# Kernel tuning notes

Hardware: AMD Instinct MI355X
Metric: run time of the kernel (lower is better)

Reference implementation:

```python
import jax, jax.numpy as jnp
import numpy as np

# Dims: N batch, I input channels, C = in/hidden/attention/projection/out channels (all 128),
# streams=1, groups=1, spatial kernel 3, dropout 0.
N, I, C, H, W = 8, 128, 128, 36, 36


def _conv(x, w, pad):
    # x: [N, Cin, H, W], w: [Cout, Cin, kh, kw]
    return jax.lax.conv_general_dilated(
        x, w, (1, 1), pad, dimension_numbers=("NCHW", "OIHW", "NCHW"))


def _bias(b):
    return b[None, :, None, None]


def setup_inputs() -> dict:
    key = jax.random.key(0)
    ks = jax.random.split(key, 16)
    std = 0.05

    def w(k, o, i, s):
        return jax.random.normal(k, (o, i, s, s), jnp.float32) * std

    p = {}
    p["inp"] = jax.random.normal(ks[0], (N, I, H, W), jnp.float32)
    p["c0"] = jax.random.normal(ks[1], (1, C, 1, 1), jnp.float32)
    # proj_x: 1x1 conv input->in_channels, bias init 0
    p["w_x"] = w(ks[2], C, I, 1)
    p["b_x"] = jnp.zeros((C,), jnp.float32)
    # token convs (3x3, no bias); q uses SAME pad, k/v VALID
    p["w_qx"] = w(ks[3], C, C, 3)
    p["w_qc"] = w(ks[4], C, C, 3)
    scale = C ** (-0.5)  # gain = attn_channels^-0.5 on k projections
    p["w_kx"] = w(ks[5], C, C, 3) * scale
    p["w_kc"] = w(ks[6], C, C, 3) * scale
    p["w_vx"] = w(ks[7], C, C, 3)
    p["w_vc"] = w(ks[8], C, C, 3)
    # gating 1x1 convs: proj_z (bias=init_gate=1), proj_n (bias=0), in 2*proj channels
    p["w_z"] = w(ks[9], C, 2 * C, 1)
    p["b_z"] = jnp.ones((C,), jnp.float32)
    p["w_n"] = w(ks[10], C, 2 * C, 1)
    p["b_n"] = jnp.zeros((C,), jnp.float32)
    # proj_h: in_channels + 2*projection_channels -> hidden
    p["w_h"] = w(ks[11], C, 3 * C, 1)
    p["b_h"] = jnp.zeros((C,), jnp.float32)
    # output 1x1 conv hidden -> out_channels
    p["w_o"] = w(ks[12], C, C, 1)
    p["b_o"] = jnp.zeros((C,), jnp.float32)
    return p


def reference(inp, c0, w_x, b_x, w_qx, w_qc, w_kx, w_kc, w_vx, w_vc,
              w_z, b_z, w_n, b_n, w_h, b_h, w_o, b_o):
    # proj_x (1x1) -> x: [N, C, H, W]
    x = _conv(inp, w_x, "VALID") + _bias(b_x)
    n_, _, hh, ww = x.shape
    c = jnp.broadcast_to(c0, (n_, c0.shape[1], hh, ww))
    q_len = hh * ww
    # q: SAME pad -> Q = H*W tokens; k/v: VALID -> D = (H-2)*(W-2) tokens
    q = jnp.stack([_conv(x, w_qx, "SAME"), _conv(c, w_qc, "SAME")], 0)
    q = q.reshape(2, n_, -1, q_len)                      # [A, N, C, Q]
    k_x = _conv(x, w_kx, "VALID")
    d_len = k_x.shape[2] * k_x.shape[3]
    k = jnp.stack([k_x, _conv(c, w_kc, "VALID")], 0).reshape(2, n_, -1, d_len)   # [B, N, C, D]
    v = jnp.stack([_conv(x, w_vx, "VALID"), _conv(c, w_vc, "VALID")], 0)
    v = v.reshape(2, n_, -1, d_len)                      # [B, N, C, D]
    # all (A query source) x (B key/value source) attention pairs
    attn = jax.nn.softmax(jnp.einsum("ancq,bncd->anbqd", q, k), axis=-1)
    a = jnp.einsum("bncd,anbqd->anbcq", v, attn)         # [A, N, B, C, Q]
    a = a.reshape(2, n_, -1, hh, ww)                     # channels = B*C = 2*proj
    a_x, a_c = a[0], a[1]
    # GRU-style gated cell update (stored state; not part of the returned output)
    z = jax.nn.sigmoid(_conv(a_c, w_z, "VALID") + _bias(b_z))
    n_cand = jnp.tanh(_conv(a_c, w_n, "VALID") + _bias(b_n))
    c_new = z * c + (1.0 - z) * n_cand  # noqa: F841 (past['c'] in the original)
    # hidden: tanh(proj_h(cat[x, a_x])), dropout p=0 is identity
    xa = jnp.concatenate([x, a_x], axis=1)               # [N, 3*C, H, W]
    h = jnp.tanh(_conv(xa, w_h, "VALID") + _bias(b_h))
    return _conv(h, w_o, "VALID") + _bias(b_o)           # [N, C, H, W]
```

## Files before the change

### kernel.cpp

```cpp
#include <hip/hip_runtime.h>
#include <hip/hip_bf16.h>
#include <math.h>

#define NN 8
#define CH 128
#define HH 36
#define WWI 36
#define PP 1296
#define DD 1156
#define VP 1280
#define KC 1152
#define QT 81
#define DT 10

typedef __attribute__((ext_vector_type(8))) short short8;
typedef __attribute__((ext_vector_type(4))) float f32x4;

__device__ inline unsigned short f2bf(float f) {
    __hip_bfloat16 h = __float2bfloat16(f);
    return __builtin_bit_cast(unsigned short, h);
}
__device__ inline float fast_tanh(float x) {
    float e = __expf(2.f * x);
    return 1.f - 2.f / (e + 1.f);
}
#define MFMA(a, b, c) __builtin_amdgcn_mfma_f32_16x16x32_bf16((a), (b), (c), 0, 0, 0)

__global__ void k_setup(const float* __restrict__ wq, const float* __restrict__ wk,
                        const float* __restrict__ wv, const float* __restrict__ wh,
                        const float* __restrict__ wo, const float* __restrict__ wx,
                        const float* __restrict__ c0, const float* __restrict__ w_vc,
                        const float* __restrict__ b_h,
                        unsigned short* __restrict__ wcat, unsigned short* __restrict__ whb,
                        unsigned short* __restrict__ wob, unsigned short* __restrict__ wxb,
                        float* __restrict__ hconst)
{
    if (blockIdx.x == 576) {
        __shared__ float vc[CH];
        int c = threadIdx.x;
        if (c < CH) {
            float s = 0.f;
            for (int ci = 0; ci < CH; ++ci) {
                const float* wp = w_vc + ((size_t)c * CH + ci) * 9;
                float ws = 0.f;
#pragma unroll
                for (int k = 0; k < 9; ++k) ws += wp[k];
                s += c0[ci] * ws;
            }
            vc[c] = s;
        }
        __syncthreads();
        if (c < CH) {
            float hs = b_h[c];
            for (int ci = 0; ci < CH; ++ci) hs += wh[(size_t)c * 384 + 256 + ci] * vc[ci];
            hconst[c] = hs;
        }
        return;
    }
    int t = blockIdx.x * 256 + threadIdx.x;
    int co = t / KC;
    int rem = t - co * KC;
    int tap = rem >> 7, ci = rem & 127;
    int iidx = co * KC + ci * 9 + tap;
    wcat[t] = f2bf(wq[iidx]);
    wcat[147456 + t] = f2bf(wk[iidx]);
    wcat[294912 + t] = f2bf(wv[iidx]);
    if (t < 32768) {
        int c2 = t >> 8, k2 = t & 255;
        whb[t] = f2bf(wh[c2 * 384 + k2]);
    }
    if (t < 16384) { wob[t] = f2bf(wo[t]); wxb[t] = f2bf(wx[t]); }
}

__global__ __launch_bounds__(64)
void k_proj(const float* __restrict__ inp, const unsigned short* __restrict__ wxb,
            const float* __restrict__ bx, unsigned short* __restrict__ xt)
{
    const int lane = threadIdx.x;
    const int quad = lane >> 4, lrow = lane & 15;
    const int p0 = blockIdx.x * 16;
    const int co0 = blockIdx.y * 64;
    const int n = blockIdx.z;
    const float* in_n = inp + (size_t)n * CH * PP;
    f32x4 acc[4] = {};

#pragma unroll
    for (int ks = 0; ks < 4; ++ks) {
        union { short8 v; unsigned short u[8]; } a;
        int ci0 = ks * 32 + quad * 8;
#pragma unroll
        for (int j = 0; j < 8; ++j)
            a.u[j] = f2bf(in_n[(size_t)(ci0 + j) * PP + p0 + lrow]);
#pragma unroll
        for (int ni = 0; ni < 4; ++ni) {
            short8 b = *(const short8*)&wxb[(size_t)(co0 + ni * 16 + lrow) * CH + ks * 32 + quad * 8];
            acc[ni] = MFMA(a.v, b, acc[ni]);
        }
    }
    unsigned short* xn = xt + (size_t)n * PP * CH;
#pragma unroll
    for (int ni = 0; ni < 4; ++ni) {
        float bv = bx[co0 + ni * 16 + lrow];
#pragma unroll
        for (int r = 0; r < 4; ++r)
            xn[(size_t)(p0 + quad * 4 + r) * CH + co0 + ni * 16 + lrow] = f2bf(acc[ni][r] + bv);
    }
}

__global__ __launch_bounds__(256)
void k_conv(const unsigned short* __restrict__ xt, const unsigned short* __restrict__ wcat,
            unsigned short* __restrict__ qt, unsigned short* __restrict__ kt,
            unsigned short* __restrict__ vb)
{
    __shared__ unsigned short lA[2][64 * 40];
    __shared__ unsigned short lB[2][128 * 40];
    const int t = threadIdx.x;
    const int wave = t >> 6, lane = t & 63;
    const int quad = lane >> 4, lrow = lane & 15;
    const int mode = blockIdx.y;
    const int n = blockIdx.z;
    const int limit = (mode == 0) ? PP : DD;
    const int tile0 = blockIdx.x * 64;
    if (tile0 >= limit) return;
    const unsigned short* xn = xt + (size_t)n * PP * CH;
    const unsigned short* wb = wcat + (size_t)mode * 128 * KC;

    const int arow = t >> 2, aseg = t & 3;
    int apr, apc;
    {
        int tok = tile0 + arow; if (tok >= limit) tok = limit - 1;
        int dv = (mode == 0) ? 36 : 34;
        apr = tok / dv; apc = tok - apr * dv;
    }

    uint4 ra, rb0, rb1;
    auto loadChunk = [&](int ks) {
        int tap = ks >> 2;
        int ky = tap / 3, kx = tap - ky * 3;
        int ci = (ks & 3) * 32 + aseg * 8;
        if (mode == 0) {
            int yy = apr + ky - 1, xx = apc + kx - 1;
            bool ok = (yy >= 0) && (yy < HH) && (xx >= 0) && (xx < WWI);
            ra = make_uint4(0, 0, 0, 0);
            if (ok) ra = *(const uint4*)&xn[(size_t)(yy * WWI + xx) * CH + ci];
        } else {
            int yy = apr + ky, xx = apc + kx;
            ra = *(const uint4*)&xn[(size_t)(yy * WWI + xx) * CH + ci];
        }
        rb0 = *(const uint4*)&wb[(size_t)arow * KC + ks * 32 + aseg * 8];
        rb1 = *(const uint4*)&wb[(size_t)(arow + 64) * KC + ks * 32 + aseg * 8];
    };
    auto storeChunk = [&](int buf) {
        *(uint4*)&lA[buf][arow * 40 + aseg * 8] = ra;
        *(uint4*)&lB[buf][arow * 40 + aseg * 8] = rb0;
        *(uint4*)&lB[buf][(arow + 64) * 40 + aseg * 8] = rb1;
    };

    f32x4 acc[4][2] = {};
    loadChunk(0);
    storeChunk(0);
    __syncthreads();

#pragma unroll
    for (int ks = 0; ks < 36; ++ks) {
        const int buf = ks & 1;
        if (ks < 35) loadChunk(ks + 1);
        short8 b0 = *(const short8*)&lB[buf][((wave * 2) * 16 + lrow) * 40 + quad * 8];
        short8 b1 = *(const short8*)&lB[buf][((wave * 2 + 1) * 16 + lrow) * 40 + quad * 8];
#pragma unroll
        for (int mi = 0; mi < 4; ++mi) {
            short8 a = *(const short8*)&lA[buf][(mi * 16 + lrow) * 40 + quad * 8];
            acc[mi][0] = MFMA(a, b0, acc[mi][0]);
            acc[mi][1] = MFMA(a, b1, acc[mi][1]);
        }
        if (ks < 35) storeChunk(buf ^ 1);
        __syncthreads();
    }

    if (mode == 0) {
        unsigned short* qn = qt + (size_t)n * PP * CH;
#pragma unroll
        for (int mi = 0; mi < 4; ++mi)
#pragma unroll
            for (int r = 0; r < 4; ++r) {
                int p = tile0 + mi * 16 + quad * 4 + r;
                if (p < PP)
#pragma unroll
                    for (int ni = 0; ni < 2; ++ni)
                        qn[(size_t)p * CH + (wave * 2 + ni) * 16 + lrow] = f2bf(acc[mi][ni][r]);
            }
    } else if (mode == 1) {
        unsigned short* kn = kt + (size_t)n * DD * CH;
#pragma unroll
        for (int mi = 0; mi < 4; ++mi)
#pragma unroll
            for (int r = 0; r < 4; ++r) {
                int d = tile0 + mi * 16 + quad * 4 + r;
                if (d < DD)
#pragma unroll
                    for (int ni = 0; ni < 2; ++ni)
                        kn[(size_t)d * CH + (wave * 2 + ni) * 16 + lrow] = f2bf(acc[mi][ni][r]);
            }
    } else {
        unsigned short* vn = vb + (size_t)n * CH * VP;
#pragma unroll
        for (int mi = 0; mi < 4; ++mi)
#pragma unroll
            for (int r = 0; r < 4; ++r) {
                int d = tile0 + mi * 16 + quad * 4 + r;
                if (d < DD)
#pragma unroll
                    for (int ni = 0; ni < 2; ++ni)
                        vn[(size_t)((wave * 2 + ni) * 16 + lrow) * VP + d] = f2bf(acc[mi][ni][r]);
            }
    }
}

__global__ __launch_bounds__(256)
void k_attn(const unsigned short* __restrict__ qt, const unsigned short* __restrict__ kt,
            const unsigned short* __restrict__ vb, _Float16* __restrict__ po,
            float* __restrict__ pm, float* __restrict__ pl)
{
    __shared__ unsigned short lS[2][128 * 40];
    __shared__ unsigned short lp[4][16 * 136];
    const int t = threadIdx.x;
    const int wave = t >> 6, lane = t & 63;
    const int quad = lane >> 4, lrow = lane & 15;
    const int qg = blockIdx.x;
    const int dt = blockIdx.y;
    const int n = blockIdx.z;
    const int qti = qg * 4 + wave;
    const int d0 = dt * 128;
    const unsigned short* qn = qt + (size_t)n * PP * CH;
    const unsigned short* kn = kt + (size_t)n * DD * CH;
    const unsigned short* vn = vb + (size_t)n * CH * VP;

    const int arow = t >> 2, aseg8 = (t & 3) * 8;
    int kr0 = d0 + arow;      if (kr0 >= DD) kr0 = DD - 1;
    int kr1 = d0 + arow + 64; if (kr1 >= DD) kr1 = DD - 1;
    const unsigned short* kp0 = kn + (size_t)kr0 * CH + aseg8;
    const unsigned short* kp1 = kn + (size_t)kr1 * CH + aseg8;
    const unsigned short* vp0 = vn + (size_t)arow * VP + d0 + aseg8;
    const unsigned short* vp1 = vn + (size_t)(arow + 64) * VP + d0 + aseg8;
    const int lo0 = arow * 40 + aseg8;
    const int lo1 = (arow + 64) * 40 + aseg8;

    short8 qa[4];
    {
        int qrow = qti * 16 + lrow; if (qrow >= PP) qrow = PP - 1;
#pragma unroll
        for (int ks = 0; ks < 4; ++ks)
            qa[ks] = *(const short8*)&qn[(size_t)qrow * CH + ks * 32 + quad * 8];
    }

    f32x4 s[8] = {};
    uint4 r0 = *(const uint4*)kp0;
    uint4 r1 = *(const uint4*)kp1;
    *(uint4*)&lS[0][lo0] = r0;
    *(uint4*)&lS[0][lo1] = r1;
    __syncthreads();
#pragma unroll
    for (int ks = 0; ks < 4; ++ks) {
        const int buf = ks & 1;
        if (ks < 3) {
            r0 = *(const uint4*)(kp0 + (ks + 1) * 32);
            r1 = *(const uint4*)(kp1 + (ks + 1) * 32);
        }
#pragma unroll
        for (int ni = 0; ni < 8; ++ni) {
            short8 b = *(const short8*)&lS[buf][(ni * 16 + lrow) * 40 + quad * 8];
            s[ni] = MFMA(qa[ks], b, s[ni]);
        }
        if (ks < 3) {
            *(uint4*)&lS[buf ^ 1][lo0] = r0;
            *(uint4*)&lS[buf ^ 1][lo1] = r1;
        }
        __syncthreads();
    }

#pragma unroll
    for (int ni = 0; ni < 8; ++ni)
        if (d0 + ni * 16 + lrow >= DD)
#pragma unroll
            for (int r = 0; r < 4; ++r) s[ni][r] = -1e30f;

    float mx[4] = {-1e30f, -1e30f, -1e30f, -1e30f};
#pragma unroll
    for (int ni = 0; ni < 8; ++ni)
#pragma unroll
        for (int r = 0; r < 4; ++r) mx[r] = fmaxf(mx[r], s[ni][r]);
#pragma unroll
    for (int off = 1; off < 16; off <<= 1)
#pragma unroll
        for (int r = 0; r < 4; ++r) mx[r] = fmaxf(mx[r], __shfl_xor(mx[r], off, 64));

    float rs[4] = {0.f, 0.f, 0.f, 0.f};
#pragma unroll
    for (int ni = 0; ni < 8; ++ni)
#pragma unroll
        for (int r = 0; r < 4; ++r) {
            float e = __expf(s[ni][r] - mx[r]);
            s[ni][r] = e;
            rs[r] += e;
        }
#pragma unroll
    for (int off = 1; off < 16; off <<= 1)
#pragma unroll
        for (int r = 0; r < 4; ++r) rs[r] += __shfl_xor(rs[r], off, 64);

#pragma unroll
    for (int ni = 0; ni < 8; ++ni)
#pragma unroll
        for (int r = 0; r < 4; ++r)
            lp[wave][(quad * 4 + r) * 136 + ni * 16 + lrow] = f2bf(s[ni][r]);

    f32x4 o[8] = {};
    r0 = *(const uint4*)vp0;
    r1 = *(const uint4*)vp1;
    *(uint4*)&lS[0][lo0] = r0;
    *(uint4*)&lS[0][lo1] = r1;
    __syncthreads();
#pragma unroll
    for (int ks = 0; ks < 4; ++ks) {
        const int buf = ks & 1;
        if (ks < 3) {
            r0 = *(const uint4*)(vp0 + (ks + 1) * 32);
            r1 = *(const uint4*)(vp1 + (ks + 1) * 32);
        }
        short8 pa = *(const short8*)&lp[wave][lrow * 136 + ks * 32 + quad * 8];
#pragma unroll
        for (int ni = 0; ni < 8; ++ni) {
            short8 b = *(const short8*)&lS[buf][(ni * 16 + lrow) * 40 + quad * 8];
            o[ni] = MFMA(pa, b, o[ni]);
        }
        if (ks < 3) {
            *(uint4*)&lS[buf ^ 1][lo0] = r0;
            *(uint4*)&lS[buf ^ 1][lo1] = r1;
        }
        __syncthreads();
    }

    if (qti < QT) {
        const int base = (n * QT + qti) * DT + dt;
        _Float16* pob = po + (size_t)base * 2048;
#pragma unroll
        for (int ni = 0; ni < 8; ++ni)
#pragma unroll
            for (int r = 0; r < 4; ++r)
                pob[(quad * 4 + r) * 128 + ni * 16 + lrow] = (_Float16)o[ni][r];
        if (lrow == 0)
#pragma unroll
            for (int r = 0; r < 4; ++r) {
                pm[base * 16 + quad * 4 + r] = mx[r];
                pl[base * 16 + quad * 4 + r] = rs[r];
            }
    }
}

__global__ __launch_bounds__(256)
void k_ahout(const _Float16* __restrict__ po, const float* __restrict__ pm,
             const float* __restrict__ pl, const unsigned short* __restrict__ xt,
             const unsigned short* __restrict__ whb, const float* __restrict__ hconst,
             const unsigned short* __restrict__ wob, const float* __restrict__ bo,
             float* __restrict__ out)
{
    __shared__ float sm[160], ssc[160], smg[16], sli[16];
    __shared__ unsigned short la0[16 * 136];
    __shared__ unsigned short lh[16 * 136];
    const int qti = blockIdx.x;
    const int n = blockIdx.y;
    const int base = (n * QT + qti) * DT;
    const int t = threadIdx.x;

    if (t < 160) sm[t] = pm[base * 16 + t];
    __syncthreads();
    if (t < 16) {
        float mg = -1e30f;
#pragma unroll
        for (int dt = 0; dt < DT; ++dt) mg = fmaxf(mg, sm[dt * 16 + t]);
        float ls = 0.f;
#pragma unroll
        for (int dt = 0; dt < DT; ++dt) ls += __expf(sm[dt * 16 + t] - mg) * pl[base * 16 + dt * 16 + t];
        smg[t] = mg; sli[t] = 1.f / ls;
    }
    __syncthreads();
    if (t < 160) ssc[t] = __expf(sm[t] - smg[t & 15]);
    __syncthreads();
#pragma unroll
    for (int k = 0; k < 8; ++k) {
        int idx = t + k * 256;
        int row = idx >> 7, c = idx & 127;
        float acc = 0.f;
#pragma unroll
        for (int dt = 0; dt < DT; ++dt)
            acc += ssc[dt * 16 + row] * (float)po[(size_t)(base + dt) * 2048 + idx];
        la0[row * 136 + c] = f2bf(acc * sli[row]);
    }
    __syncthreads();

    const int wave = t >> 6, lane = t & 63;
    const int quad = lane >> 4, lrow = lane & 15;
    const int p0 = qti * 16;
    const unsigned short* x0 = xt + (size_t)n * PP * CH;

    f32x4 acc1[2] = {};
#pragma unroll
    for (int ks = 0; ks < 8; ++ks) {
        int col = (ks & 3) * 32 + quad * 8;
        short8 a;
        if (ks < 4) a = *(const short8*)&x0[(size_t)(p0 + lrow) * CH + col];
        else        a = *(const short8*)&la0[lrow * 136 + col];
#pragma unroll
        for (int j = 0; j < 2; ++j) {
            int ni = wave * 2 + j;
            short8 b = *(const short8*)&whb[(size_t)(ni * 16 + lrow) * 256 + ks * 32 + quad * 8];
            acc1[j] = MFMA(a, b, acc1[j]);
        }
    }
#pragma unroll
    for (int j = 0; j < 2; ++j) {
        int ni = wave * 2 + j;
        float hc = hconst[ni * 16 + lrow];
#pragma unroll
        for (int r = 0; r < 4; ++r)
            lh[(quad * 4 + r) * 136 + ni * 16 + lrow] = f2bf(fast_tanh(acc1[j][r] + hc));
    }
    __syncthreads();

    f32x4 acc2[2] = {};
#pragma unroll
    for (int ks = 0; ks < 4; ++ks) {
        short8 a = *(const short8*)&lh[lrow * 136 + ks * 32 + quad * 8];
#pragma unroll
        for (int j = 0; j < 2; ++j) {
            int ni = wave * 2 + j;
            short8 b = *(const short8*)&wob[(size_t)(ni * 16 + lrow) * CH + ks * 32 + quad * 8];
            acc2[j] = MFMA(a, b, acc2[j]);
        }
    }
#pragma unroll
    for (int j = 0; j < 2; ++j) {
        int ni = wave * 2 + j;
        float bv = bo[ni * 16 + lrow];
#pragma unroll
        for (int r = 0; r < 4; ++r)
            out[((size_t)(n * CH + ni * 16 + lrow)) * PP + p0 + quad * 4 + r] = acc2[j][r] + bv;
    }
}

extern "C" void kernel_launch(void* const* d_in, const int* in_sizes, int n_in,
                              void* d_out, int out_size, void* d_ws, size_t ws_size,
                              hipStream_t stream)
{
    const float* inp  = (const float*)d_in[0];
    const float* c0   = (const float*)d_in[1];
    const float* w_x  = (const float*)d_in[2];
    const float* b_x  = (const float*)d_in[3];
    const float* w_qx = (const float*)d_in[4];
    const float* w_kx = (const float*)d_in[6];
    const float* w_vx = (const float*)d_in[8];
    const float* w_vc = (const float*)d_in[9];
    const float* w_h  = (const float*)d_in[14];
    const float* b_h  = (const float*)d_in[15];
    const float* w_o  = (const float*)d_in[16];
    const float* b_o  = (const float*)d_in[17];
    float* out = (float*)d_out;

    char* w = (char*)d_ws;
    unsigned short* xt   = (unsigned short*)(w);
    unsigned short* qt   = (unsigned short*)(w + 2654208);
    unsigned short* kt   = (unsigned short*)(w + 5308416);
    unsigned short* vb   = (unsigned short*)(w + 7675904);
    unsigned short* wcat = (unsigned short*)(w + 12951552);
    unsigned short* wxb  = (unsigned short*)(w + 13836288);
    unsigned short* whb  = (unsigned short*)(w + 13869056);
    unsigned short* wob  = (unsigned short*)(w + 13934592);
    float* hconst        = (float*)(w + 13967360);
    float* pm            = (float*)(w + 13967872);
    float* pl            = (float*)(w + 14382592);
    _Float16* po         = (_Float16*)(w + 14797312);

    hipLaunchKernelGGL(k_setup, dim3(577), dim3(256), 0, stream,
                       w_qx, w_kx, w_vx, w_h, w_o, w_x, c0, w_vc, b_h,
                       wcat, whb, wob, wxb, hconst);

    hipLaunchKernelGGL(k_proj, dim3(QT, 2, NN), dim3(64), 0, stream, inp, wxb, b_x, xt);

    hipLaunchKernelGGL(k_conv, dim3(21, 3, NN), dim3(256), 0, stream, xt, wcat, qt, kt, vb);

    hipLaunchKernelGGL(k_attn, dim3(21, DT, NN), dim3(256), 0, stream, qt, kt, vb, po, pm, pl);

    hipLaunchKernelGGL(k_ahout, dim3(QT, NN), dim3(256), 0, stream,
                       po, pm, pl, xt, whb, hconst, wob, b_o, out);
}
```

Measured before the change: 198.3 us.

## Process two key tiles per attention block with online softmax, halving partials

Each attention block now covers 256 keys in two 128-key halves, merging them with an online-softmax rescale of the running max, sum and output accumulator. This halves the number of partial outputs written to global memory and reduced in the merge kernel, whose buffers shrink accordingly. The setup kernel's constant-hidden-bias computation is also parallelised across 256 threads with vectorised loads. The cost is fewer attention blocks with longer serial work each, which may reduce parallelism on the GPU.

```diff
diff --git a/kernel.cpp b/kernel.cpp
--- a/kernel.cpp
+++ b/kernel.cpp
@@ -11,7 +11,7 @@
 #define VP 1280
 #define KC 1152
 #define QT 81
-#define DT 10
+#define DT 5
 
 typedef __attribute__((ext_vector_type(8))) short short8;
 typedef __attribute__((ext_vector_type(4))) float f32x4;
@@ -36,25 +36,41 @@
                         float* __restrict__ hconst)
 {
     if (blockIdx.x == 576) {
-        __shared__ float vc[CH];
-        int c = threadIdx.x;
-        if (c < CH) {
+        __shared__ float c0s[CH];
+        __shared__ float part[256];
+        __shared__ float vcs[CH];
+        const int t = threadIdx.x;
+        const int c = t & 127, half = t >> 7;
+        if (t < CH) c0s[t] = c0[t];
+        __syncthreads();
+        {
+            const float* row = w_vc + (size_t)c * 1152 + half * 576;
             float s = 0.f;
-            for (int ci = 0; ci < CH; ++ci) {
-                const float* wp = w_vc + ((size_t)c * CH + ci) * 9;
-                float ws = 0.f;
-#pragma unroll
-                for (int k = 0; k < 9; ++k) ws += wp[k];
-                s += c0[ci] * ws;
-            }
-            vc[c] = s;
-        }
-        __syncthreads();
-        if (c < CH) {
-            float hs = b_h[c];
-            for (int ci = 0; ci < CH; ++ci) hs += wh[(size_t)c * 384 + 256 + ci] * vc[ci];
-            hconst[c] = hs;
-        }
+#pragma unroll 4
+            for (int j4 = 0; j4 < 144; ++j4) {
+                float4 v = ((const float4*)row)[j4];
+                int j = half * 576 + j4 * 4;
+                s += v.x * c0s[j / 9] + v.y * c0s[(j + 1) / 9]
+                   + v.z * c0s[(j + 2) / 9] + v.w * c0s[(j + 3) / 9];
+            }
+            part[t] = s;
+        }
+        __syncthreads();
+        if (t < CH) vcs[t] = part[t] + part[t + 128];
+        __syncthreads();
+        {
+            const float* wrow = wh + (size_t)c * 384 + 256 + half * 64;
+            float hs = 0.f;
+#pragma unroll
+            for (int j4 = 0; j4 < 16; ++j4) {
+                float4 v = ((const float4*)wrow)[j4];
+                int ci = half * 64 + j4 * 4;
+                hs += v.x * vcs[ci] + v.y * vcs[ci + 1] + v.z * vcs[ci + 2] + v.w * vcs[ci + 3];
+            }
+            part[t] = hs;
+        }
+        __syncthreads();
+        if (t < CH) hconst[t] = b_h[t] + part[t] + part[t + 128];
         return;
     }
     int t = blockIdx.x * 256 + threadIdx.x;
@@ -230,18 +246,12 @@
     const int dt = blockIdx.y;
     const int n = blockIdx.z;
     const int qti = qg * 4 + wave;
-    const int d0 = dt * 128;
+    const int d0 = dt * 256;
     const unsigned short* qn = qt + (size_t)n * PP * CH;
     const unsigned short* kn = kt + (size_t)n * DD * CH;
     const unsigned short* vn = vb + (size_t)n * CH * VP;
 
     const int arow = t >> 2, aseg8 = (t & 3) * 8;
-    int kr0 = d0 + arow;      if (kr0 >= DD) kr0 = DD - 1;
-    int kr1 = d0 + arow + 64; if (kr1 >= DD) kr1 = DD - 1;
-    const unsigned short* kp0 = kn + (size_t)kr0 * CH + aseg8;
-    const unsigned short* kp1 = kn + (size_t)kr1 * CH + aseg8;
-    const unsigned short* vp0 = vn + (size_t)arow * VP + d0 + aseg8;
-    const unsigned short* vp1 = vn + (size_t)(arow + 64) * VP + d0 + aseg8;
     const int lo0 = arow * 40 + aseg8;
     const int lo1 = (arow + 64) * 40 + aseg8;
 
@@ -253,91 +263,121 @@
             qa[ks] = *(const short8*)&qn[(size_t)qrow * CH + ks * 32 + quad * 8];
     }
 
-    f32x4 s[8] = {};
-    uint4 r0 = *(const uint4*)kp0;
-    uint4 r1 = *(const uint4*)kp1;
-    *(uint4*)&lS[0][lo0] = r0;
-    *(uint4*)&lS[0][lo1] = r1;
-    __syncthreads();
-#pragma unroll
-    for (int ks = 0; ks < 4; ++ks) {
-        const int buf = ks & 1;
-        if (ks < 3) {
-            r0 = *(const uint4*)(kp0 + (ks + 1) * 32);
-            r1 = *(const uint4*)(kp1 + (ks + 1) * 32);
-        }
-#pragma unroll
-        for (int ni = 0; ni < 8; ++ni) {
-            short8 b = *(const short8*)&lS[buf][(ni * 16 + lrow) * 40 + quad * 8];
-            s[ni] = MFMA(qa[ks], b, s[ni]);
-        }
-        if (ks < 3) {
-            *(uint4*)&lS[buf ^ 1][lo0] = r0;
-            *(uint4*)&lS[buf ^ 1][lo1] = r1;
-        }
-        __syncthreads();
-    }
-
-#pragma unroll
-    for (int ni = 0; ni < 8; ++ni)
-        if (d0 + ni * 16 + lrow >= DD)
-#pragma unroll
-            for (int r = 0; r < 4; ++r) s[ni][r] = -1e30f;
-
+    f32x4 o[8] = {};
     float mx[4] = {-1e30f, -1e30f, -1e30f, -1e30f};
-#pragma unroll
-    for (int ni = 0; ni < 8; ++ni)
-#pragma unroll
-        for (int r = 0; r < 4; ++r) mx[r] = fmaxf(mx[r], s[ni][r]);
-#pragma unroll
-    for (int off = 1; off < 16; off <<= 1)
-#pragma unroll
-        for (int r = 0; r < 4; ++r) mx[r] = fmaxf(mx[r], __shfl_xor(mx[r], off, 64));
-
     float rs[4] = {0.f, 0.f, 0.f, 0.f};
-#pragma unroll
-    for (int ni = 0; ni < 8; ++ni)
+
+#pragma unroll
+    for (int h = 0; h < 2; ++h) {
+        const int dbase = d0 + h * 128;
+        int kr0 = dbase + arow;      if (kr0 >= DD) kr0 = DD - 1;
+        int kr1 = dbase + arow + 64; if (kr1 >= DD) kr1 = DD - 1;
+        const unsigned short* kp0 = kn + (size_t)kr0 * CH + aseg8;
+        const unsigned short* kp1 = kn + (size_t)kr1 * CH + aseg8;
+        const unsigned short* vp0 = vn + (size_t)arow * VP + dbase + aseg8;
+        const unsigned short* vp1 = vn + (size_t)(arow + 64) * VP + dbase + aseg8;
+
+        f32x4 s[8] = {};
+        uint4 r0 = *(const uint4*)kp0;
+        uint4 r1 = *(const uint4*)kp1;
+        *(uint4*)&lS[0][lo0] = r0;
+        *(uint4*)&lS[0][lo1] = r1;
+        __syncthreads();
+#pragma unroll
+        for (int ks = 0; ks < 4; ++ks) {
+            const int buf = ks & 1;
+            if (ks < 3) {
+                r0 = *(const uint4*)(kp0 + (ks + 1) * 32);
+                r1 = *(const uint4*)(kp1 + (ks + 1) * 32);
+            }
+#pragma unroll
+            for (int ni = 0; ni < 8; ++ni) {
+                short8 b = *(const short8*)&lS[buf][(ni * 16 + lrow) * 40 + quad * 8];
+                s[ni] = MFMA(qa[ks], b, s[ni]);
+            }
+            if (ks < 3) {
+                *(uint4*)&lS[buf ^ 1][lo0] = r0;
+                *(uint4*)&lS[buf ^ 1][lo1] = r1;
+            }
+            __syncthreads();
+        }
+
+#pragma unroll
+        for (int ni = 0; ni < 8; ++ni)
+            if (dbase + ni * 16 + lrow >= DD)
+#pragma unroll
+                for (int r = 0; r < 4; ++r) s[ni][r] = -1e30f;
+
+        float hm[4] = {-1e30f, -1e30f, -1e30f, -1e30f};
+#pragma unroll
+        for (int ni = 0; ni < 8; ++ni)
+#pragma unroll
+            for (int r = 0; r < 4; ++r) hm[r] = fmaxf(hm[r], s[ni][r]);
+#pragma unroll
+        for (int off = 1; off < 16; off <<= 1)
+#pragma unroll
+            for (int r = 0; r < 4; ++r) hm[r] = fmaxf(hm[r], __shfl_xor(hm[r], off, 64));
+
+        float m[4], sc[4];
 #pragma unroll
         for (int r = 0; r < 4; ++r) {
-            float e = __expf(s[ni][r] - mx[r]);
-            s[ni][r] = e;
-            rs[r] += e;
-        }
-#pragma unroll
-    for (int off = 1; off < 16; off <<= 1)
-#pragma unroll
-        for (int r = 0; r < 4; ++r) rs[r] += __shfl_xor(rs[r], off, 64);
-
-#pragma unroll
-    for (int ni = 0; ni < 8; ++ni)
-#pragma unroll
-        for (int r = 0; r < 4; ++r)
-            lp[wave][(quad * 4 + r) * 136 + ni * 16 + lrow] = f2bf(s[ni][r]);
-
-    f32x4 o[8] = {};
-    r0 = *(const uint4*)vp0;
-    r1 = *(const uint4*)vp1;
-    *(uint4*)&lS[0][lo0] = r0;
-    *(uint4*)&lS[0][lo1] = r1;
-    __syncthreads();
-#pragma unroll
-    for (int ks = 0; ks < 4; ++ks) {
-        const int buf = ks & 1;
-        if (ks < 3) {
-            r0 = *(const uint4*)(vp0 + (ks + 1) * 32);
-            r1 = *(const uint4*)(vp1 + (ks + 1) * 32);
-        }
-        short8 pa = *(const short8*)&lp[wave][lrow * 136 + ks * 32 + quad * 8];
-#pragma unroll
-        for (int ni = 0; ni < 8; ++ni) {
-            short8 b = *(const short8*)&lS[buf][(ni * 16 + lrow) * 40 + quad * 8];
-            o[ni] = MFMA(pa, b, o[ni]);
-        }
-        if (ks < 3) {
-            *(uint4*)&lS[buf ^ 1][lo0] = r0;
-            *(uint4*)&lS[buf ^ 1][lo1] = r1;
-        }
-        __syncthreads();
+            m[r] = fmaxf(mx[r], hm[r]);
+            sc[r] = __expf(mx[r] - m[r]);
+        }
+
+        float hs[4] = {0.f, 0.f, 0.f, 0.f};
+#pragma unroll
+        for (int ni = 0; ni < 8; ++ni)
+#pragma unroll
+            for (int r = 0; r < 4; ++r) {
+                float e = __expf(s[ni][r] - m[r]);
+                s[ni][r] = e;
+                hs[r] += e;
+            }
+#pragma unroll
+        for (int off = 1; off < 16; off <<= 1)
+#pragma unroll
+            for (int r = 0; r < 4; ++r) hs[r] += __shfl_xor(hs[r], off, 64);
+#pragma unroll
+        for (int r = 0; r < 4; ++r) {
+            rs[r] = rs[r] * sc[r] + hs[r];
+            mx[r] = m[r];
+        }
+#pragma unroll
+        for (int ni = 0; ni < 8; ++ni)
+#pragma unroll
+            for (int r = 0; r < 4; ++r) o[ni][r] *= sc[r];
+
+#pragma unroll
+        for (int ni = 0; ni < 8; ++ni)
+#pragma unroll
+            for (int r = 0; r < 4; ++r)
+                lp[wave][(quad * 4 + r) * 136 + ni * 16 + lrow] = f2bf(s[ni][r]);
+
+        r0 = *(const uint4*)vp0;
+        r1 = *(const uint4*)vp1;
+        *(uint4*)&lS[0][lo0] = r0;
+        *(uint4*)&lS[0][lo1] = r1;
+        __syncthreads();
+#pragma unroll
+        for (int ks = 0; ks < 4; ++ks) {
+            const int buf = ks & 1;
+            if (ks < 3) {
+                r0 = *(const uint4*)(vp0 + (ks + 1) * 32);
+                r1 = *(const uint4*)(vp1 + (ks + 1) * 32);
+            }
+            short8 pa = *(const short8*)&lp[wave][lrow * 136 + ks * 32 + quad * 8];
+#pragma unroll
+            for (int ni = 0; ni < 8; ++ni) {
+                short8 b = *(const short8*)&lS[buf][(ni * 16 + lrow) * 40 + quad * 8];
+                o[ni] = MFMA(pa, b, o[ni]);
+            }
+            if (ks < 3) {
+                *(uint4*)&lS[buf ^ 1][lo0] = r0;
+                *(uint4*)&lS[buf ^ 1][lo1] = r1;
+            }
+            __syncthreads();
+        }
     }
 
     if (qti < QT) {
@@ -364,7 +404,7 @@
              const unsigned short* __restrict__ wob, const float* __restrict__ bo,
              float* __restrict__ out)
 {
-    __shared__ float sm[160], ssc[160], smg[16], sli[16];
+    __shared__ float sm[80], ssc[80], smg[16], sli[16];
     __shared__ unsigned short la0[16 * 136];
     __shared__ unsigned short lh[16 * 136];
     const int qti = blockIdx.x;
@@ -372,7 +412,7 @@
     const int base = (n * QT + qti) * DT;
     const int t = threadIdx.x;
 
-    if (t < 160) sm[t] = pm[base * 16 + t];
+    if (t < 80) sm[t] = pm[base * 16 + t];
     __syncthreads();
     if (t < 16) {
         float mg = -1e30f;
@@ -384,7 +424,7 @@
         smg[t] = mg; sli[t] = 1.f / ls;
     }
     __syncthreads();
-    if (t < 160) ssc[t] = __expf(sm[t] - smg[t & 15]);
+    if (t < 80) ssc[t] = __expf(sm[t] - smg[t & 15]);
     __syncthreads();
 #pragma unroll
     for (int k = 0; k < 8; ++k) {
```

After: 192.7 us. -2.9%, faster.
